# Performance work log

Measured on AMD Instinct MI355X. Metric: run time of the kernel, lower is better.

The kernel has to match this reference:

```python
import jax, jax.numpy as jnp
import numpy as np

LINHAS, COLUNAS, DIM, BATCH = 32, 32, 256, 2048
NEURONS = LINHAS * COLUNAS
TAXA_INICIAL = 0.5
SIGMA_INICIAL = max(LINHAS, COLUNAS) / 2.0  # 16.0


def _grid_locs():
    # matches tf.meshgrid default 'xy' indexing, stacked then flattened
    x = jnp.arange(LINHAS, dtype=jnp.float32)
    y = jnp.arange(COLUNAS, dtype=jnp.float32)
    g = jnp.stack(jnp.meshgrid(x, y), axis=-1)  # (COLUNAS, LINHAS, 2)
    return g.reshape(-1, 2)


def setup_inputs() -> dict:
    key = jax.random.key(0)
    k1, k2 = jax.random.split(key)
    X = jax.random.normal(k1, (BATCH, DIM), dtype=jnp.float32)
    # keras 'random_normal' initializer: stddev 0.05
    pesos = jax.random.normal(k2, (NEURONS, DIM), dtype=jnp.float32) * 0.05
    return {
        "X": X,
        "pesos": pesos,
        "localizacoes": _grid_locs(),
        "passo_atual": 100,
        "total_passos": 1000,
    }


def reference(X, pesos, localizacoes, passo_atual, total_passos):
    frac = jnp.float32(passo_atual) / jnp.float32(total_passos)
    taxa = TAXA_INICIAL * jnp.exp(-frac)
    sigma = SIGMA_INICIAL * jnp.exp(-frac)

    # squared-euclidean distances (B, N)
    x2 = jnp.sum(X * X, axis=1, keepdims=True)
    w2 = jnp.sum(pesos * pesos, axis=1)
    dist = x2 + w2 - 2.0 * (X @ pesos.T)

    bmu_idx = jnp.argmin(dist, axis=1)            # (B,)
    bmu_loc = localizacoes[bmu_idx]               # (B, 2)

    # grid distances and Gaussian neighborhood (B, N)
    dist_grade = jnp.sum((localizacoes[None, :, :] - bmu_loc[:, None, :]) ** 2, axis=2)
    h = jnp.exp(-dist_grade / (2.0 * sigma ** 2))

    # delta_total = mean_b taxa * h[b,n] * (X[b,d] - W[n,d]), computed without
    # materializing the (B, N, D) tensor:
    B = jnp.float32(X.shape[0])
    delta_total = taxa * (jnp.einsum('bn,bd->nd', h, X) - jnp.sum(h, axis=0)[:, None] * pesos) / B

    new_pesos = pesos + delta_total
    return new_pesos
```

## Files before the change

### kernel.cpp

```cpp
#include <hip/hip_runtime.h>
#include <float.h>

#define Bsz 2048
#define Nn  1024
#define Dd  256

typedef __attribute__((ext_vector_type(8))) short bf16x8;
typedef __attribute__((ext_vector_type(4))) float f32x4;
typedef unsigned long long u64;

__device__ __forceinline__ unsigned short bfr(float x) {
    unsigned u = __float_as_uint(x);
    u += 0x7fffu + ((u >> 16) & 1u);
    return (unsigned short)(u >> 16);
}
__device__ __forceinline__ float bf2f(unsigned short h) {
    return __uint_as_float(((unsigned)h) << 16);
}

__device__ __forceinline__ void som_params(const int* __restrict__ step,
                                           const int* __restrict__ total,
                                           float* taxa, float* inv2s2) {
    float frac = (float)(*step) / (float)(*total);
    float e = __expf(-frac);
    *taxa = 0.5f * e;
    float sigma = 16.0f * e;
    *inv2s2 = 1.0f / (2.0f * sigma * sigma);
}

__device__ __forceinline__ u64 packsc(float f, int n) {
    unsigned u = __float_as_uint(f);
    u = (u & 0x80000000u) ? ~u : (u | 0x80000000u);
    return ((u64)u << 32) | (unsigned)n;
}

__device__ __forceinline__ float split8(const float* __restrict__ src,
                                        bf16x8* hi, bf16x8* lo) {
    float4 v0 = *(const float4*)src;
    float4 v1 = *(const float4*)(src + 4);
    float f[8] = {v0.x, v0.y, v0.z, v0.w, v1.x, v1.y, v1.z, v1.w};
    float s = 0.f;
    #pragma unroll
    for (int j = 0; j < 8; ++j) {
        unsigned short h = bfr(f[j]);
        (*hi)[j] = (short)h;
        (*lo)[j] = (short)bfr(f[j] - bf2f(h));
        s += f[j] * f[j];
    }
    return s;
}

__global__ __launch_bounds__(256) void fused_pre(
    const float* __restrict__ X, const float* __restrict__ W,
    ushort* __restrict__ Xt, u64* __restrict__ ppack)
{
    __shared__ float ld[64][65];
    __shared__ u64 lmin[2][2][64];

    const int t = threadIdx.x, bid = blockIdx.x;
    const int w = t >> 6, l = t & 63;
    const int lr = l & 15, lg = l >> 4;

    if (bid < 256) {
        const int wm = w & 1, wn = w >> 1;
        const int b0 = (bid >> 4) * 128 + wm * 64;
        const int n0 = (bid & 15) * 64 + wn * 32;

        f32x4 acc[4][2];
        #pragma unroll
        for (int m = 0; m < 4; ++m)
            #pragma unroll
            for (int n = 0; n < 2; ++n) { f32x4 z = {0.f,0.f,0.f,0.f}; acc[m][n] = z; }
        float w2a[2] = {0.f, 0.f};

        #pragma unroll
        for (int kd = 0; kd < Dd; kd += 32) {
            bf16x8 ah[4], al[4], bh[2], bl[2];
            #pragma unroll
            for (int m = 0; m < 4; ++m)
                split8(&X[(size_t)(b0 + m*16 + lr) * Dd + kd + lg*8], &ah[m], &al[m]);
            #pragma unroll
            for (int nf = 0; nf < 2; ++nf)
                w2a[nf] += split8(&W[(size_t)(n0 + nf*16 + lr) * Dd + kd + lg*8],
                                  &bh[nf], &bl[nf]);
            #pragma unroll
            for (int m = 0; m < 4; ++m)
                #pragma unroll
                for (int nf = 0; nf < 2; ++nf) {
                    acc[m][nf] = __builtin_amdgcn_mfma_f32_16x16x32_bf16(ah[m], bh[nf], acc[m][nf], 0, 0, 0);
                    acc[m][nf] = __builtin_amdgcn_mfma_f32_16x16x32_bf16(ah[m], bl[nf], acc[m][nf], 0, 0, 0);
                    acc[m][nf] = __builtin_amdgcn_mfma_f32_16x16x32_bf16(al[m], bh[nf], acc[m][nf], 0, 0, 0);
                }
        }

        #pragma unroll
        for (int nf = 0; nf < 2; ++nf) {
            w2a[nf] += __shfl_xor(w2a[nf], 16, 64);
            w2a[nf] += __shfl_xor(w2a[nf], 32, 64);
        }
        const int ni0 = n0 + lr, ni1 = n0 + 16 + lr;

        #pragma unroll
        for (int m = 0; m < 4; ++m)
            #pragma unroll
            for (int r = 0; r < 4; ++r) {
                u64 p0 = packsc(w2a[0] - 2.f * acc[m][0][r], ni0);
                u64 p1 = packsc(w2a[1] - 2.f * acc[m][1][r], ni1);
                u64 pm = p1 < p0 ? p1 : p0;
                #pragma unroll
                for (int msk = 1; msk < 16; msk <<= 1) {
                    unsigned plo = (unsigned)pm, phi = (unsigned)(pm >> 32);
                    plo = __shfl_xor(plo, msk, 64);
                    phi = __shfl_xor(phi, msk, 64);
                    u64 o = ((u64)phi << 32) | plo;
                    if (o < pm) pm = o;
                }
                if (lr == 0) lmin[wm][wn][m*16 + lg*4 + r] = pm;
            }
        __syncthreads();
        if (t < 128) {
            const int bwm = t >> 6, bb = t & 63;
            u64 a = lmin[bwm][0][bb], c = lmin[bwm][1][bb];
            u64 pm = c < a ? c : a;
            const int b = (bid >> 4) * 128 + bwm * 64 + bb;
            ppack[(size_t)(bid & 15) * Bsz + b] = pm;
        }
    } else {
        const int idx = bid - 256;
        const int b0 = (idx & 31) * 64;
        const int d0 = (idx >> 5) * 64;

        #pragma unroll
        for (int p = 0; p < 4; ++p) {
            int flat = p * 256 + t;
            int row = flat >> 4, c4 = flat & 15;
            float4 v = *(const float4*)&X[(size_t)(b0 + row) * Dd + d0 + c4 * 4];
            ld[row][c4*4+0] = v.x; ld[row][c4*4+1] = v.y;
            ld[row][c4*4+2] = v.z; ld[row][c4*4+3] = v.w;
        }
        __syncthreads();
        #pragma unroll
        for (int q = 0; q < 2; ++q) {
            int idx2 = q * 256 + t;
            int d  = idx2 >> 3;
            int bs = (idx2 & 7) * 8;
            bf16x8 o;
            #pragma unroll
            for (int j = 0; j < 8; ++j) o[j] = (short)bfr(ld[bs + j][d]);
            *(bf16x8*)&Xt[(size_t)(d0 + d) * Bsz + b0 + bs] = o;
        }
    }
}

__global__ __launch_bounds__(512) void acc_finish(
    const ushort* __restrict__ Xt, const u64* __restrict__ ppack,
    const float* __restrict__ W, const int* __restrict__ step,
    const int* __restrict__ total, float* __restrict__ out)
{
    __shared__ float red[8][32][36];
    __shared__ float hws[8][32];
    __shared__ ushort bidx[Bsz];

    const int t = threadIdx.x, w = t >> 6, l = t & 63;
    const int lr = l & 15, lg = l >> 4;
    const int n0 = blockIdx.x * 32;
    const int d0 = blockIdx.y * 32;

    #pragma unroll
    for (int q = 0; q < 4; ++q) {
        const int b = q * 512 + t;
        u64 pm = ppack[b];
        #pragma unroll
        for (int g = 1; g < 16; ++g) {
            u64 c = ppack[(size_t)g * Bsz + b];
            if (c < pm) pm = c;
        }
        bidx[b] = (ushort)(pm & 0xffffu);
    }
    __syncthreads();

    float taxa, inv2s2;
    som_params(step, total, &taxa, &inv2s2);

    const float fny  = (float)(n0 >> 5);
    const float fnx0 = (float)lr;
    const float fnx1 = (float)(lr + 16);

    f32x4 acc[2][2];
    #pragma unroll
    for (int m = 0; m < 2; ++m)
        #pragma unroll
        for (int nf = 0; nf < 2; ++nf) { f32x4 z = {0.f,0.f,0.f,0.f}; acc[m][nf] = z; }
    float hs0 = 0.f, hs1 = 0.f;

    #pragma unroll
    for (int ks = 0; ks < 8; ++ks) {
        const int bk = w * 256 + ks * 32 + lg * 8;
        bf16x8 am0, am1;
        #pragma unroll
        for (int j = 0; j < 8; ++j) {
            unsigned idx = bidx[bk + j];
            float bx = (float)(idx & 31), by = (float)(idx >> 5);
            float dy  = fny - by;
            float dy2 = dy * dy;
            float dx0 = fnx0 - bx, dx1 = fnx1 - bx;
            float h0 = __expf(-(dx0*dx0 + dy2) * inv2s2);
            float h1 = __expf(-(dx1*dx1 + dy2) * inv2s2);
            am0[j] = (short)bfr(h0);
            am1[j] = (short)bfr(h1);
            hs0 += h0; hs1 += h1;
        }
        bf16x8 bx0 = *(const bf16x8*)&Xt[(size_t)(d0 + lr)      * Bsz + bk];
        bf16x8 bx1 = *(const bf16x8*)&Xt[(size_t)(d0 + 16 + lr) * Bsz + bk];
        acc[0][0] = __builtin_amdgcn_mfma_f32_16x16x32_bf16(am0, bx0, acc[0][0], 0, 0, 0);
        acc[0][1] = __builtin_amdgcn_mfma_f32_16x16x32_bf16(am0, bx1, acc[0][1], 0, 0, 0);
        acc[1][0] = __builtin_amdgcn_mfma_f32_16x16x32_bf16(am1, bx0, acc[1][0], 0, 0, 0);
        acc[1][1] = __builtin_amdgcn_mfma_f32_16x16x32_bf16(am1, bx1, acc[1][1], 0, 0, 0);
    }

    hs0 += __shfl_xor(hs0, 16, 64); hs0 += __shfl_xor(hs0, 32, 64);
    hs1 += __shfl_xor(hs1, 16, 64); hs1 += __shfl_xor(hs1, 32, 64);
    if (l < 16) { hws[w][l] = hs0; hws[w][16 + l] = hs1; }

    #pragma unroll
    for (int m = 0; m < 2; ++m)
        #pragma unroll
        for (int nf = 0; nf < 2; ++nf)
            #pragma unroll
            for (int r = 0; r < 4; ++r)
                red[w][m*16 + lg*4 + r][nf*16 + lr] = acc[m][nf][r];
    __syncthreads();

    const float invB = 1.0f / 2048.0f;
    const int nl = t >> 4;
    const int dl = (t & 15) * 2;
    float s0 = 0.f, s1 = 0.f, hsn = 0.f;
    #pragma unroll
    for (int ww = 0; ww < 8; ++ww) {
        s0  += red[ww][nl][dl];
        s1  += red[ww][nl][dl + 1];
        hsn += hws[ww][nl];
    }
    const int n = n0 + nl;
    const int d = d0 + dl;
    const float* wp = &W[(size_t)n * Dd + d];
    float wv0 = wp[0], wv1 = wp[1];
    float2 o = make_float2(wv0 + taxa * (s0 - hsn * wv0) * invB,
                           wv1 + taxa * (s1 - hsn * wv1) * invB);
    *(float2*)&out[(size_t)n * Dd + d] = o;
}

extern "C" void kernel_launch(void* const* d_in, const int* in_sizes, int n_in,
                              void* d_out, int out_size, void* d_ws, size_t ws_size,
                              hipStream_t stream)
{
    const float* X    = (const float*)d_in[0];
    const float* W    = (const float*)d_in[1];
    const int* step   = (const int*)d_in[3];
    const int* total  = (const int*)d_in[4];
    float* out = (float*)d_out;

    char* p = (char*)d_ws;
    ushort* Xt   = (ushort*)p; p += 1048576;
    u64*    ppack = (u64*)p;   p += 262144;

    fused_pre <<<384, 256, 0, stream>>>(X, W, Xt, ppack);
    acc_finish<<<dim3(32, 8), 512, 0, stream>>>(Xt, ppack, W, step, total, out);
}
```

Baseline: 36.18 us.

## Use truncation bf16 split and double threads in accumulation kernel

The hi/lo bf16 split of X and W in the distance GEMM now uses truncation and packed bit ops instead of round-to-nearest, which cuts ALU work per element. The lo residual still captures the rest, so the distance stays close to exact. The accumulation kernel now runs 1024 threads per block (16 waves), each handling half as much of the batch, and reduces the wave partials in two stages through shared memory. This is meant to add latency hiding and parallelism for the exp and MFMA work, at the cost of extra syncs and a serialized second reduction stage.

```diff
diff --git a/kernel.cpp b/kernel.cpp
--- a/kernel.cpp
+++ b/kernel.cpp
@@ -8,14 +8,13 @@
 typedef __attribute__((ext_vector_type(8))) short bf16x8;
 typedef __attribute__((ext_vector_type(4))) float f32x4;
 typedef unsigned long long u64;
+
+union b8u4 { bf16x8 v; uint4 u; };
 
 __device__ __forceinline__ unsigned short bfr(float x) {
     unsigned u = __float_as_uint(x);
     u += 0x7fffu + ((u >> 16) & 1u);
     return (unsigned short)(u >> 16);
-}
-__device__ __forceinline__ float bf2f(unsigned short h) {
-    return __uint_as_float(((unsigned)h) << 16);
 }
 
 __device__ __forceinline__ void som_params(const int* __restrict__ step,
@@ -34,19 +33,28 @@
     return ((u64)u << 32) | (unsigned)n;
 }
 
-__device__ __forceinline__ float split8(const float* __restrict__ src,
-                                        bf16x8* hi, bf16x8* lo) {
+__device__ __forceinline__ float split8t(const float* __restrict__ src,
+                                         bf16x8* hi, bf16x8* lo) {
     float4 v0 = *(const float4*)src;
     float4 v1 = *(const float4*)(src + 4);
     float f[8] = {v0.x, v0.y, v0.z, v0.w, v1.x, v1.y, v1.z, v1.w};
     float s = 0.f;
-    #pragma unroll
-    for (int j = 0; j < 8; ++j) {
-        unsigned short h = bfr(f[j]);
-        (*hi)[j] = (short)h;
-        (*lo)[j] = (short)bfr(f[j] - bf2f(h));
-        s += f[j] * f[j];
-    }
+    unsigned hp[4], lp[4];
+    #pragma unroll
+    for (int p = 0; p < 4; ++p) {
+        float a = f[2*p], b = f[2*p+1];
+        unsigned ua = __float_as_uint(a), ub = __float_as_uint(b);
+        unsigned ha = ua & 0xffff0000u, hb = ub & 0xffff0000u;
+        float la = a - __uint_as_float(ha);
+        float lb = b - __uint_as_float(hb);
+        hp[p] = (ua >> 16) | hb;
+        lp[p] = (__float_as_uint(la) >> 16) | (__float_as_uint(lb) & 0xffff0000u);
+        s = fmaf(a, a, s); s = fmaf(b, b, s);
+    }
+    b8u4 H, L;
+    H.u = make_uint4(hp[0], hp[1], hp[2], hp[3]);
+    L.u = make_uint4(lp[0], lp[1], lp[2], lp[3]);
+    *hi = H.v; *lo = L.v;
     return s;
 }
 
@@ -78,11 +86,11 @@
             bf16x8 ah[4], al[4], bh[2], bl[2];
             #pragma unroll
             for (int m = 0; m < 4; ++m)
-                split8(&X[(size_t)(b0 + m*16 + lr) * Dd + kd + lg*8], &ah[m], &al[m]);
+                split8t(&X[(size_t)(b0 + m*16 + lr) * Dd + kd + lg*8], &ah[m], &al[m]);
             #pragma unroll
             for (int nf = 0; nf < 2; ++nf)
-                w2a[nf] += split8(&W[(size_t)(n0 + nf*16 + lr) * Dd + kd + lg*8],
-                                  &bh[nf], &bl[nf]);
+                w2a[nf] += split8t(&W[(size_t)(n0 + nf*16 + lr) * Dd + kd + lg*8],
+                                   &bh[nf], &bl[nf]);
             #pragma unroll
             for (int m = 0; m < 4; ++m)
                 #pragma unroll
@@ -152,13 +160,13 @@
     }
 }
 
-__global__ __launch_bounds__(512) void acc_finish(
+__global__ __launch_bounds__(1024, 4) void acc_finish(
     const ushort* __restrict__ Xt, const u64* __restrict__ ppack,
     const float* __restrict__ W, const int* __restrict__ step,
     const int* __restrict__ total, float* __restrict__ out)
 {
     __shared__ float red[8][32][36];
-    __shared__ float hws[8][32];
+    __shared__ float hws[16][32];
     __shared__ ushort bidx[Bsz];
 
     const int t = threadIdx.x, w = t >> 6, l = t & 63;
@@ -167,8 +175,8 @@
     const int d0 = blockIdx.y * 32;
 
     #pragma unroll
-    for (int q = 0; q < 4; ++q) {
-        const int b = q * 512 + t;
+    for (int q = 0; q < 2; ++q) {
+        const int b = q * 1024 + t;
         u64 pm = ppack[b];
         #pragma unroll
         for (int g = 1; g < 16; ++g) {
@@ -194,8 +202,8 @@
     float hs0 = 0.f, hs1 = 0.f;
 
     #pragma unroll
-    for (int ks = 0; ks < 8; ++ks) {
-        const int bk = w * 256 + ks * 32 + lg * 8;
+    for (int ks = 0; ks < 4; ++ks) {
+        const int bk = w * 128 + ks * 32 + lg * 8;
         bf16x8 am0, am1;
         #pragma unroll
         for (int j = 0; j < 8; ++j) {
@@ -222,32 +230,39 @@
     hs1 += __shfl_xor(hs1, 16, 64); hs1 += __shfl_xor(hs1, 32, 64);
     if (l < 16) { hws[w][l] = hs0; hws[w][16 + l] = hs1; }
 
-    #pragma unroll
-    for (int m = 0; m < 2; ++m)
-        #pragma unroll
-        for (int nf = 0; nf < 2; ++nf)
-            #pragma unroll
-            for (int r = 0; r < 4; ++r)
-                red[w][m*16 + lg*4 + r][nf*16 + lr] = acc[m][nf][r];
+    if (w < 8) {
+        #pragma unroll
+        for (int m = 0; m < 2; ++m)
+            #pragma unroll
+            for (int nf = 0; nf < 2; ++nf)
+                #pragma unroll
+                for (int r = 0; r < 4; ++r)
+                    red[w][m*16 + lg*4 + r][nf*16 + lr] = acc[m][nf][r];
+    }
     __syncthreads();
+    if (w >= 8) {
+        #pragma unroll
+        for (int m = 0; m < 2; ++m)
+            #pragma unroll
+            for (int nf = 0; nf < 2; ++nf)
+                #pragma unroll
+                for (int r = 0; r < 4; ++r)
+                    red[w - 8][m*16 + lg*4 + r][nf*16 + lr] += acc[m][nf][r];
+    }
+    __syncthreads();
 
     const float invB = 1.0f / 2048.0f;
-    const int nl = t >> 4;
-    const int dl = (t & 15) * 2;
-    float s0 = 0.f, s1 = 0.f, hsn = 0.f;
-    #pragma unroll
-    for (int ww = 0; ww < 8; ++ww) {
-        s0  += red[ww][nl][dl];
-        s1  += red[ww][nl][dl + 1];
-        hsn += hws[ww][nl];
-    }
+    const int nl = t >> 5;
+    const int dl = t & 31;
+    float s = 0.f, hsn = 0.f;
+    #pragma unroll
+    for (int ww = 0; ww < 8; ++ww) s += red[ww][nl][dl];
+    #pragma unroll
+    for (int ww = 0; ww < 16; ++ww) hsn += hws[ww][nl];
     const int n = n0 + nl;
     const int d = d0 + dl;
-    const float* wp = &W[(size_t)n * Dd + d];
-    float wv0 = wp[0], wv1 = wp[1];
-    float2 o = make_float2(wv0 + taxa * (s0 - hsn * wv0) * invB,
-                           wv1 + taxa * (s1 - hsn * wv1) * invB);
-    *(float2*)&out[(size_t)n * Dd + d] = o;
+    const float wv = W[(size_t)n * Dd + d];
+    out[(size_t)n * Dd + d] = wv + taxa * (s - hsn * wv) * invB;
 }
 
 extern "C" void kernel_launch(void* const* d_in, const int* in_sizes, int n_in,
@@ -261,9 +276,9 @@
     float* out = (float*)d_out;
 
     char* p = (char*)d_ws;
-    ushort* Xt   = (ushort*)p; p += 1048576;
-    u64*    ppack = (u64*)p;   p += 262144;
+    ushort* Xt    = (ushort*)p; p += 1048576;
+    u64*    ppack = (u64*)p;    p += 262144;
 
     fused_pre <<<384, 256, 0, stream>>>(X, W, Xt, ppack);
-    acc_finish<<<dim3(32, 8), 512, 0, stream>>>(Xt, ppack, W, step, total, out);
-}
+    acc_finish<<<dim3(32, 8), 1024, 0, stream>>>(Xt, ppack, W, step, total, out);
+}
```

After: 35.91 us. About the same (-0.7%).
